# Kernel optimization log

Measured on AMD Instinct MI355X. Metric: run time of the kernel, lower is better.

Reference implementation:

```python
import jax, jax.numpy as jnp
import numpy as np

B, K = 16, 50
IN_CH, N_CLASSES, N_ANCH = 256, 80, 3
STRIDE, FSIZE, IGNORE_THRE = 8, 76, 0.7
N_CH = 5 + N_CLASSES
ANCHORS = np.array([[10,13],[16,30],[33,23],[30,61],[62,45],[59,119],[116,90],[156,198],[373,326]], np.float32)
ALL_GRID = ANCHORS / STRIDE            # all 9 anchors in grid units
ANCH_MASK = np.array([0, 1, 2])        # layer_no = 2
MASKED = ALL_GRID[ANCH_MASK]           # (3,2) anchors used by this head


def setup_inputs():
    key = jax.random.key(0)
    k1, k2, k3, k4, k5, k6 = jax.random.split(key, 6)
    xin = jax.random.normal(k1, (B, IN_CH, FSIZE, FSIZE), jnp.float32)
    cls = jax.random.randint(k2, (B, K), 0, N_CLASSES).astype(jnp.float32)
    xy = jax.random.uniform(k3, (B, K, 2), minval=0.05, maxval=0.95)
    wh = jax.random.uniform(k4, (B, K, 2), minval=0.02, maxval=0.30)
    labels = jnp.concatenate([cls[..., None], xy, wh], -1)   # (B,K,5) [cls,xc,yc,w,h]
    oc = N_ANCH * N_CH
    conv_w = jax.random.normal(k5, (oc, IN_CH), jnp.float32) * 0.01
    conv_b = jax.random.normal(k6, (oc,), jnp.float32) * 0.01
    return {"xin": xin, "labels": labels, "conv_w": conv_w, "conv_b": conv_b}


def _yolo(xin, conv_w, conv_b, labels):
    f, C = FSIZE, N_CLASSES
    # 1x1 conv == channel matmul
    raw = jnp.einsum('bchw,oc->bohw', xin, conv_w) + conv_b[None, :, None, None]
    raw = raw.reshape(B, N_ANCH, N_CH, f, f).transpose(0, 1, 3, 4, 2)  # (B,A,f,f,85)
    # sigmoid on x,y,obj,cls; w,h stay raw
    out = jnp.concatenate([jax.nn.sigmoid(raw[..., :2]), raw[..., 2:4], jax.nn.sigmoid(raw[..., 4:])], -1)

    grid = jnp.arange(f, dtype=jnp.float32)
    mw = jnp.asarray(MASKED[:, 0]); mh = jnp.asarray(MASKED[:, 1])
    px = out[..., 0] + grid[None, None, None, :]
    py = out[..., 1] + grid[None, None, :, None]
    pw = jnp.exp(out[..., 2]) * mw[None, :, None, None]
    ph = jnp.exp(out[..., 3]) * mh[None, :, None, None]
    pred = jax.lax.stop_gradient(jnp.stack([px, py, pw, ph], -1))  # detached, like torch .data

    labels = jax.lax.stop_gradient(labels)
    valid = labels.sum(-1) > 0                  # (B,K) padding rows are all-zero
    tx = labels[..., 1] * f; ty = labels[..., 2] * f
    tw = labels[..., 3] * f; th = labels[..., 4] * f
    ii = tx.astype(jnp.int32); jj = ty.astype(jnp.int32)

    # anchor matching: IoU of [0,0,w,h] truth vs [0,0,aw,ah] ref anchors (corners at origin)
    aw = jnp.asarray(ALL_GRID[:, 0]); ah = jnp.asarray(ALL_GRID[:, 1])
    inter_a = jnp.minimum(tw[..., None], aw) * jnp.minimum(th[..., None], ah)  # (B,K,9)
    iou_a = inter_a / (tw[..., None] * th[..., None] + aw * ah - inter_a)
    best_n_all = jnp.argmax(iou_a, -1)
    best_n = best_n_all % 3
    best_mask = (best_n_all == ANCH_MASK[0]) | (best_n_all == ANCH_MASK[1]) | (best_n_all == ANCH_MASK[2])

    # pred-vs-truth IoU in cxcywh form (xyxy=False)
    pa = pred.reshape(B, -1, 4)                 # (B, A*f*f, 4)
    tb = jnp.stack([tx, ty, tw, th], -1)        # (B, K, 4)
    tl = jnp.maximum(pa[:, :, None, :2] - pa[:, :, None, 2:] * 0.5, tb[:, None, :, :2] - tb[:, None, :, 2:] * 0.5)
    br = jnp.minimum(pa[:, :, None, :2] + pa[:, :, None, 2:] * 0.5, tb[:, None, :, :2] + tb[:, None, :, 2:] * 0.5)
    en = jnp.all(tl < br, -1)
    inter = jnp.prod(br - tl, -1) * en
    area_p = pa[..., 2] * pa[..., 3]; area_t = tb[..., 2] * tb[..., 3]
    iou_p = inter / (area_p[:, :, None] + area_t[:, None, :] - inter)
    iou_p = jnp.where(valid[:, None, :], iou_p, 0.0)
    ignore = (iou_p.max(-1) > IGNORE_THRE).reshape(B, N_ANCH, f, f)
    obj_mask = 1.0 - ignore.astype(jnp.float32)

    # scatter positive targets; non-selected rows routed out-of-bounds and dropped
    sel = valid & best_mask
    bb = jnp.where(sel, jnp.arange(B)[:, None], B)
    obj_mask = obj_mask.at[bb, best_n, jj, ii].set(1.0, mode='drop')
    tgt_mask = jnp.zeros((B, N_ANCH, f, f, 4 + C)).at[bb, best_n, jj, ii].set(1.0, mode='drop')
    scale = jnp.sqrt(2.0 - tw * th / (f * f))
    tgt_scale = jnp.zeros((B, N_ANCH, f, f, 2)).at[bb, best_n, jj, ii].set(
        jnp.broadcast_to(scale[..., None], (B, K, 2)), mode='drop')
    tvals = jnp.concatenate([
        (tx - ii)[..., None], (ty - jj)[..., None],
        jnp.log(tw / mw[best_n] + 1e-16)[..., None],
        jnp.log(th / mh[best_n] + 1e-16)[..., None],
        jnp.ones((B, K, 1), jnp.float32),
        jax.nn.one_hot(labels[..., 0].astype(jnp.int32), C)], -1)  # (B,K,85)
    target = jnp.zeros((B, N_ANCH, f, f, N_CH)).at[bb, best_n, jj, ii].set(tvals, mode='drop')

    oxy = out[..., :2] * tgt_mask[..., :2]
    owh = out[..., 2:4] * tgt_mask[..., 2:4] * tgt_scale
    oob = out[..., 4] * obj_mask
    ocl = out[..., 5:] * tgt_mask[..., 4:]
    txy = target[..., :2] * tgt_mask[..., :2]
    twh = target[..., 2:4] * tgt_mask[..., 2:4] * tgt_scale
    tob = target[..., 4] * obj_mask
    tcl = target[..., 5:] * tgt_mask[..., 4:]

    def bce(p, t, w=None):
        pc = jnp.clip(p, 1e-12, 1.0 - 1e-7)
        e = -(t * jnp.log(pc) + (1.0 - t) * jnp.log(1.0 - pc))
        if w is not None:
            e = e * w
        return e.sum()

    loss_xy = bce(oxy, txy, tgt_scale * tgt_scale)
    loss_wh = 0.5 * jnp.sum((owh - twh) ** 2)
    loss_obj = bce(oob, tob)
    loss_cls = bce(ocl, tcl)
    out_m = jnp.concatenate([oxy, owh, oob[..., None], ocl], -1)
    tgt_m = jnp.concatenate([txy, twh, tob[..., None], tcl], -1)
    loss_l2 = jnp.sum((out_m - tgt_m) ** 2)
    loss = loss_xy + loss_wh + loss_obj + loss_cls
    return loss, loss_xy, loss_wh, loss_obj, loss_cls, loss_l2, out_m


def reference(xin, labels, conv_w, conv_b):
    return _yolo(xin, conv_w, conv_b, labels)
```

## Files before the change

kernel.cpp:

```cpp
#include <hip/hip_runtime.h>
#include <hip/hip_bf16.h>

#define B_   16
#define K_   50
#define CIN  256
#define F_   76
#define A_   3
#define NCH  85
#define OC   255
#define HW   (F_*F_)
#define NBLK (B_*F_)
#define NCELL (A_*F_)
#define SLAB (F_*NCH)

#define WS_BIAS_F 32768
#define WS_LAB_F  33024
#define WS_PART_F 45824
#define WS_W15_F  55552

typedef __attribute__((ext_vector_type(8))) short short8;
typedef __attribute__((ext_vector_type(4))) float f32x4;

__device__ __constant__ float AW9[9] = {1.25f, 2.0f, 4.125f, 3.75f, 7.75f, 7.375f, 14.5f, 19.5f, 46.625f};
__device__ __constant__ float AH9[9] = {1.625f, 3.75f, 2.875f, 7.625f, 5.625f, 14.875f, 11.25f, 24.75f, 40.75f};

__device__ __forceinline__ unsigned short f2bf(float f) {
    union { float f; unsigned int u; } v; v.f = f;
    unsigned int r = v.u + 0x7fffu + ((v.u >> 16) & 1u);
    return (unsigned short)(r >> 16);
}
__device__ __forceinline__ float bf2f(unsigned short b) {
    union { unsigned int u; float f; } v; v.u = ((unsigned int)b) << 16;
    return v.f;
}
__device__ __forceinline__ float sigm(float r) { return 1.0f / (1.0f + __expf(-r)); }
__device__ __forceinline__ float bce_t(float p, float tv) {
    float pc = fminf(fmaxf(p, 1e-12f), 1.0f - 1e-7f);
    return -(tv * __logf(pc) + (1.0f - tv) * __logf(1.0f - pc));
}

__global__ void prep_kernel(const float* __restrict__ conv_w, const float* __restrict__ conv_b,
                            const float* __restrict__ labels, float* __restrict__ ws) {
    int bid = blockIdx.x, t = threadIdx.x;
    if (bid < 256) {
        float v = (t < OC) ? conv_w[t * CIN + bid] : 0.0f;
        ((unsigned short*)ws)[bid * 256 + t] = f2bf(v);
    } else if (bid == 256) {
        ws[WS_BIAS_F + t] = (t < OC) ? conv_b[t] : 0.0f;
    } else if (bid == 257) {
        for (int idx = t; idx < B_ * K_; idx += 256) {
            const float* L = labels + idx * 5;
            float cls = L[0], xc = L[1], yc = L[2], wl = L[3], hl = L[4];
            float ssum = cls + xc + yc + wl + hl;
            float validf = (ssum > 0.0f) ? 1.0f : 0.0f;
            float tx = xc * F_, ty = yc * F_, tw = wl * F_, th = hl * F_;
            int ii = (int)tx, jj = (int)ty;
            float tarea = tw * th;
            float best = -1.0f; int bn = 0;
            #pragma unroll
            for (int n = 0; n < 9; n++) {
                float inter = fminf(tw, AW9[n]) * fminf(th, AH9[n]);
                float iou = inter / (tarea + AW9[n] * AH9[n] - inter);
                if (iou > best) { best = iou; bn = n; }
            }
            int a = bn % 3;
            bool self = (validf != 0.0f) && (bn < 3);
            float* R = ws + WS_LAB_F + idx * 16;
            R[0] = tx; R[1] = ty; R[2] = tw; R[3] = th;
            R[4] = validf; R[5] = self ? (float)a : -1.0f; R[6] = (float)ii; R[7] = (float)jj;
            R[8] = tx - (float)ii; R[9] = ty - (float)jj;
            R[10] = __logf(tw / AW9[a] + 1e-16f);
            R[11] = __logf(th / AH9[a] + 1e-16f);
            R[12] = sqrtf(2.0f - tarea / (float)HW);
            R[13] = cls; R[14] = 0.0f; R[15] = 0.0f;
        }
    } else {
        unsigned short* wf = (unsigned short*)(ws + WS_W15_F);
        for (int idx = t; idx < 4096; idx += 256) {
            int ks = idx >> 9, lane = (idx >> 3) & 63, jj = idx & 7;
            int row = lane & 15;
            int k = ks * 32 + (lane >> 4) * 8 + jj;
            float v = 0.0f;
            if (row < 15) v = conv_w[((row / 5) * NCH + (row % 5)) * CIN + k];
            wf[idx] = f2bf(v);
        }
    }
}

__global__ __launch_bounds__(320) void fused_kernel(const float* __restrict__ xin,
                                                    const float* __restrict__ ws,
                                                    float* __restrict__ d_out,
                                                    float* __restrict__ part) {
    __shared__ float raw5S[15 * F_];
    __shared__ float4 LAB[K_ * 4];
    __shared__ int   flagS[NCELL];
    __shared__ float omvS[NCELL];
    __shared__ float xcolS[256];
    __shared__ float redS[5][5];

    const int t = threadIdx.x;
    const int w = t >> 6, lane = t & 63;
    const int b = blockIdx.x / F_;
    const int j = blockIdx.x % F_;
    const int lr = lane & 15, q = lane >> 4;
    const int col0 = (w < 4) ? (w << 4) : 60;

    if (t < K_ * 4) LAB[t] = ((const float4*)(ws + WS_LAB_F + b * (K_ * 16)))[t];

    const unsigned short* wf15 = (const unsigned short*)(ws + WS_W15_F);
    short8 afr[8];
    #pragma unroll
    for (int ks = 0; ks < 8; ks++)
        afr[ks] = *(const short8*)&wf15[(ks * 64 + lane) * 8];

    f32x4 acc = (f32x4){0.0f, 0.0f, 0.0f, 0.0f};
    const float* xbase = xin + (size_t)b * CIN * HW + j * F_ + col0 + lr;
    #pragma unroll
    for (int ks = 0; ks < 8; ks++) {
        int kb = ks * 32 + q * 8;
        float xv[8];
        #pragma unroll
        for (int jj = 0; jj < 8; jj++) xv[jj] = xbase[(size_t)(kb + jj) * HW];
        union { short8 s; __hip_bfloat162 h[4]; } u;
        #pragma unroll
        for (int p = 0; p < 4; p++)
            u.h[p] = __float22bfloat162_rn(make_float2(xv[2 * p], xv[2 * p + 1]));
        acc = __builtin_amdgcn_mfma_f32_16x16x32_bf16(afr[ks], u.s, acc, 0, 0, 0);
    }

    const float* biasg = ws + WS_BIAS_F;
    if (w < 4 || lr >= 4) {
        #pragma unroll
        for (int r = 0; r < 4; r++) {
            int row = q * 4 + r;
            if (row < 15) {
                int o = (row / 5) * NCH + (row % 5);
                raw5S[row * F_ + col0 + lr] = acc[r] + biasg[o];
            }
        }
    }
    __syncthreads();

    float lxy = 0.0f, lwh = 0.0f, lobj = 0.0f, lcls = 0.0f, l2 = 0.0f;
    if (t < NCELL) {
        int a = t / F_, i = t - a * F_;
        float x   = sigm(raw5S[(a * 5 + 0) * F_ + i]);
        float y   = sigm(raw5S[(a * 5 + 1) * F_ + i]);
        float wr  = raw5S[(a * 5 + 2) * F_ + i];
        float hr  = raw5S[(a * 5 + 3) * F_ + i];
        float obj = sigm(raw5S[(a * 5 + 4) * F_ + i]);

        float px = x + (float)i, py = y + (float)j;
        float pw = __expf(wr) * AW9[a], ph = __expf(hr) * AH9[a];
        float hpw = pw * 0.5f, hph = ph * 0.5f;
        float areap = pw * ph;
        float fa_t = (float)a, fi_t = (float)i, fj_t = (float)j;

        float maxiou = 0.0f; int mk = -1;
        #pragma unroll 2
        for (int k = 0; k < K_; k++) {
            float4 A0 = LAB[4 * k + 0];
            float4 A1 = LAB[4 * k + 1];
            float tx = A0.x, ty = A0.y, tw = A0.z, th = A0.w;
            float tlx = fmaxf(px - hpw, tx - tw * 0.5f);
            float tly = fmaxf(py - hph, ty - th * 0.5f);
            float brx = fminf(px + hpw, tx + tw * 0.5f);
            float bry = fminf(py + hph, ty + th * 0.5f);
            float iw = brx - tlx, ih = bry - tly;
            float inter = (iw > 0.0f && ih > 0.0f) ? iw * ih : 0.0f;
            float iou = __fdividef(inter, areap + tw * th - inter);
            iou = (A1.x != 0.0f) ? iou : 0.0f;
            maxiou = fmaxf(maxiou, iou);
            bool match = (A1.y == fa_t) & (A1.z == fi_t) & (A1.w == fj_t);
            mk = match ? k : mk;
        }
        float objmask = (maxiou > 0.7f) ? 0.0f : 1.0f;

        if (mk >= 0) {
            float4 B0 = LAB[4 * mk + 2];
            float4 B1 = LAB[4 * mk + 3];
            float sc = B1.x, sc2 = sc * sc;
            float txv = B0.x, tyv = B0.y, twv = B0.z, thv = B0.w;
            lxy = (bce_t(x, txv) + bce_t(y, tyv)) * sc2;
            float dw = wr - twv, dh = hr - thv;
            lwh = 0.5f * sc2 * (dw * dw + dh * dh);
            float pco = fminf(fmaxf(obj, 1e-12f), 1.0f - 1e-7f);
            lobj = -__logf(pco);
            float dx = x - txv, dy = y - tyv, dob = obj - 1.0f;
            l2 = dx * dx + dy * dy + sc2 * (dw * dw + dh * dh) + dob * dob;
            flagS[t] = mk + 1;
            omvS[t]  = obj;
        } else {
            float oo = obj * objmask;
            if (objmask != 0.0f) {
                float pco = fminf(obj, 1.0f - 1e-7f);
                lobj = -__logf(1.0f - pco);
            }
            l2 = oo * oo;
            flagS[t] = 0;
            omvS[t]  = oo;
        }
    }
    __syncthreads();

    for (int a = 0; a < A_; a++) {
        float2* dst = (float2*)(d_out + 6 + (size_t)((b * A_ + a) * F_ + j) * SLAB);
        for (int idx2 = t; idx2 < SLAB / 2; idx2 += 320) {
            int p = idx2 << 1;
            int i0 = p / NCH, c0 = p - i0 * NCH;
            int i1 = i0, c1 = c0 + 1;
            if (c1 == NCH) { i1++; c1 = 0; }
            float v0 = (c0 == 4) ? omvS[a * F_ + i0] : 0.0f;
            float v1 = (c1 == 4) ? omvS[a * F_ + i1] : 0.0f;
            dst[idx2] = make_float2(v0, v1);
        }
    }
    __threadfence_block();
    __syncthreads();

    const unsigned short* Wtg = (const unsigned short*)ws;
    for (int k = 0; k < K_; k++) {
        float4 A1 = LAB[4 * k + 1];
        int fa = (int)A1.y;
        if (fa < 0) continue;
        if ((int)A1.w != j) continue;
        int fi = (int)A1.z;
        int cell = fa * F_ + fi;
        if (flagS[cell] != k + 1) continue;

        if (t < 256) xcolS[t] = xin[((size_t)b * CIN + t) * HW + j * F_ + fi];
        __syncthreads();
        float4 B1 = LAB[4 * k + 3];
        float sc = B1.x; int cl = (int)B1.y;
        if (t < NCH) {
            float v; int chout;
            if (t < 80) {
                int o = fa * NCH + 5 + t;
                float accv = biasg[o];
                #pragma unroll 8
                for (int kk = 0; kk < 256; kk++)
                    accv += bf2f(Wtg[kk * 256 + o]) * xcolS[kk];
                float p = sigm(accv);
                float tcv = (t == cl) ? 1.0f : 0.0f;
                lcls += bce_t(p, tcv);
                float d = p - tcv;
                l2 += d * d;
                v = p; chout = 5 + t;
            } else {
                int ch = t - 80;
                float raw = raw5S[(fa * 5 + ch) * F_ + fi];
                v = (ch == 2 || ch == 3) ? raw * sc : sigm(raw);
                chout = ch;
            }
            d_out[6 + (size_t)((b * A_ + fa) * F_ + j) * SLAB + fi * NCH + chout] = v;
        }
        __syncthreads();
    }

    #pragma unroll
    for (int off = 32; off > 0; off >>= 1) {
        lxy  += __shfl_down(lxy, off);
        lwh  += __shfl_down(lwh, off);
        lobj += __shfl_down(lobj, off);
        lcls += __shfl_down(lcls, off);
        l2   += __shfl_down(l2, off);
    }
    if (lane == 0) {
        redS[w][0] = lxy; redS[w][1] = lwh; redS[w][2] = lobj;
        redS[w][3] = lcls; redS[w][4] = l2;
    }
    __syncthreads();
    if (t == 0) {
        float* P = part + (size_t)blockIdx.x * 8;
        #pragma unroll
        for (int q2 = 0; q2 < 5; q2++)
            P[q2] = redS[0][q2] + redS[1][q2] + redS[2][q2] + redS[3][q2] + redS[4][q2];
    }
}

__global__ void finish_kernel(const float* __restrict__ part, float* __restrict__ d_out) {
    int t = threadIdx.x;
    float s0 = 0, s1 = 0, s2 = 0, s3 = 0, s4 = 0;
    for (int bidx = t; bidx < NBLK; bidx += 256) {
        const float* P = part + (size_t)bidx * 8;
        s0 += P[0]; s1 += P[1]; s2 += P[2]; s3 += P[3]; s4 += P[4];
    }
    #pragma unroll
    for (int off = 32; off > 0; off >>= 1) {
        s0 += __shfl_down(s0, off); s1 += __shfl_down(s1, off);
        s2 += __shfl_down(s2, off); s3 += __shfl_down(s3, off);
        s4 += __shfl_down(s4, off);
    }
    __shared__ float red[4][5];
    if ((t & 63) == 0) {
        int w = t >> 6;
        red[w][0] = s0; red[w][1] = s1; red[w][2] = s2; red[w][3] = s3; red[w][4] = s4;
    }
    __syncthreads();
    if (t == 0) {
        float r0 = red[0][0] + red[1][0] + red[2][0] + red[3][0];
        float r1 = red[0][1] + red[1][1] + red[2][1] + red[3][1];
        float r2 = red[0][2] + red[1][2] + red[2][2] + red[3][2];
        float r3 = red[0][3] + red[1][3] + red[2][3] + red[3][3];
        float r4 = red[0][4] + red[1][4] + red[2][4] + red[3][4];
        d_out[0] = r0 + r1 + r2 + r3;
        d_out[1] = r0; d_out[2] = r1; d_out[3] = r2; d_out[4] = r3; d_out[5] = r4;
    }
}

extern "C" void kernel_launch(void* const* d_in, const int* in_sizes, int n_in,
                              void* d_out, int out_size, void* d_ws, size_t ws_size,
                              hipStream_t stream) {
    const float* xin    = (const float*)d_in[0];
    const float* labels = (const float*)d_in[1];
    const float* conv_w = (const float*)d_in[2];
    const float* conv_b = (const float*)d_in[3];
    float* out  = (float*)d_out;
    float* ws   = (float*)d_ws;
    float* part = ws + WS_PART_F;

    prep_kernel<<<259, 256, 0, stream>>>(conv_w, conv_b, labels, ws);
    fused_kernel<<<NBLK, 320, 0, stream>>>(xin, ws, out, part);
    finish_kernel<<<1, 256, 0, stream>>>(part, out);
}
```

Before: 212.4 us.

## Stage x row tile in LDS as bf16 with coalesced loads; simplify output zero-fill

```diff
diff --git a/kernel.cpp b/kernel.cpp
--- a/kernel.cpp
+++ b/kernel.cpp
@@ -12,6 +12,7 @@
 #define NBLK (B_*F_)
 #define NCELL (A_*F_)
 #define SLAB (F_*NCH)
+#define XPAD 78
 
 #define WS_BIAS_F 32768
 #define WS_LAB_F  33024
@@ -91,10 +92,10 @@
                                                     const float* __restrict__ ws,
                                                     float* __restrict__ d_out,
                                                     float* __restrict__ part) {
+    __shared__ unsigned short xS[256 * XPAD];
     __shared__ float raw5S[15 * F_];
     __shared__ float4 LAB[K_ * 4];
     __shared__ int   flagS[NCELL];
-    __shared__ float omvS[NCELL];
     __shared__ float xcolS[256];
     __shared__ float redS[5][5];
 
@@ -105,26 +106,43 @@
     const int lr = lane & 15, q = lane >> 4;
     const int col0 = (w < 4) ? (w << 4) : 60;
 
-    if (t < K_ * 4) LAB[t] = ((const float4*)(ws + WS_LAB_F + b * (K_ * 16)))[t];
-
     const unsigned short* wf15 = (const unsigned short*)(ws + WS_W15_F);
     short8 afr[8];
     #pragma unroll
     for (int ks = 0; ks < 8; ks++)
         afr[ks] = *(const short8*)&wf15[(ks * 64 + lane) * 8];
 
+    {
+        const float* xrow = xin + (size_t)b * CIN * HW + j * F_;
+        #pragma unroll 4
+        for (int it = 0; it < 16; ++it) {
+            int fidx = t + it * 320;
+            if (fidx < 256 * 19) {
+                int c = fidx / 19, pg = fidx - c * 19;
+                float4 v = *(const float4*)(xrow + (size_t)c * HW + pg * 4);
+                __hip_bfloat162 h0 = __float22bfloat162_rn(make_float2(v.x, v.y));
+                __hip_bfloat162 h1 = __float22bfloat162_rn(make_float2(v.z, v.w));
+                unsigned int* dst = (unsigned int*)&xS[c * XPAD + pg * 4];
+                dst[0] = *(unsigned int*)&h0;
+                dst[1] = *(unsigned int*)&h1;
+            }
+        }
+    }
+    if (t < K_ * 4) LAB[t] = ((const float4*)(ws + WS_LAB_F + b * (K_ * 16)))[t];
+    __syncthreads();
+
+    const int pp = col0 + lr;
     f32x4 acc = (f32x4){0.0f, 0.0f, 0.0f, 0.0f};
-    const float* xbase = xin + (size_t)b * CIN * HW + j * F_ + col0 + lr;
     #pragma unroll
     for (int ks = 0; ks < 8; ks++) {
         int kb = ks * 32 + q * 8;
-        float xv[8];
+        unsigned short ev[8];
         #pragma unroll
-        for (int jj = 0; jj < 8; jj++) xv[jj] = xbase[(size_t)(kb + jj) * HW];
-        union { short8 s; __hip_bfloat162 h[4]; } u;
+        for (int jj = 0; jj < 8; jj++) ev[jj] = xS[(kb + jj) * XPAD + pp];
+        union { short8 s; unsigned int d[4]; } u;
         #pragma unroll
-        for (int p = 0; p < 4; p++)
-            u.h[p] = __float22bfloat162_rn(make_float2(xv[2 * p], xv[2 * p + 1]));
+        for (int p2 = 0; p2 < 4; p2++)
+            u.d[p2] = (unsigned int)ev[2 * p2] | ((unsigned int)ev[2 * p2 + 1] << 16);
         acc = __builtin_amdgcn_mfma_f32_16x16x32_bf16(afr[ks], u.s, acc, 0, 0, 0);
     }
 
@@ -142,6 +160,7 @@
     __syncthreads();
 
     float lxy = 0.0f, lwh = 0.0f, lobj = 0.0f, lcls = 0.0f, l2 = 0.0f;
+    float omv = 0.0f;
     if (t < NCELL) {
         int a = t / F_, i = t - a * F_;
         float x   = sigm(raw5S[(a * 5 + 0) * F_ + i]);
@@ -189,7 +208,7 @@
             float dx = x - txv, dy = y - tyv, dob = obj - 1.0f;
             l2 = dx * dx + dy * dy + sc2 * (dw * dw + dh * dh) + dob * dob;
             flagS[t] = mk + 1;
-            omvS[t]  = obj;
+            omv = obj;
         } else {
             float oo = obj * objmask;
             if (objmask != 0.0f) {
@@ -198,22 +217,23 @@
             }
             l2 = oo * oo;
             flagS[t] = 0;
-            omvS[t]  = oo;
-        }
-    }
-    __syncthreads();
-
+            omv = oo;
+        }
+    }
+    __syncthreads();
+
+    #pragma unroll
     for (int a = 0; a < A_; a++) {
         float2* dst = (float2*)(d_out + 6 + (size_t)((b * A_ + a) * F_ + j) * SLAB);
-        for (int idx2 = t; idx2 < SLAB / 2; idx2 += 320) {
-            int p = idx2 << 1;
-            int i0 = p / NCH, c0 = p - i0 * NCH;
-            int i1 = i0, c1 = c0 + 1;
-            if (c1 == NCH) { i1++; c1 = 0; }
-            float v0 = (c0 == 4) ? omvS[a * F_ + i0] : 0.0f;
-            float v1 = (c1 == 4) ? omvS[a * F_ + i1] : 0.0f;
-            dst[idx2] = make_float2(v0, v1);
-        }
+        for (int idx2 = t; idx2 < SLAB / 2; idx2 += 320)
+            dst[idx2] = make_float2(0.0f, 0.0f);
+    }
+    __threadfence_block();
+    __syncthreads();
+
+    if (t < NCELL) {
+        int a = t / F_, i = t - a * F_;
+        d_out[6 + (size_t)((b * A_ + a) * F_ + j) * SLAB + i * NCH + 4] = omv;
     }
     __threadfence_block();
     __syncthreads();
```

Result: slower. 227.7 us (+7.2%).

## Pre-transpose input to channel-last bf16 in workspace and vectorize slab writes

Applied to the files above, without the earlier changes.

```diff
diff --git a/kernel.cpp b/kernel.cpp
--- a/kernel.cpp
+++ b/kernel.cpp
@@ -17,6 +17,10 @@
 #define WS_LAB_F  33024
 #define WS_PART_F 45824
 #define WS_W15_F  55552
+#define WS_XT_F   57600
+#define XT_FLOATS (11829248u)
+
+#define NTILE 91
 
 typedef __attribute__((ext_vector_type(8))) short short8;
 typedef __attribute__((ext_vector_type(4))) float f32x4;
@@ -39,8 +43,11 @@
     return -(tv * __logf(pc) + (1.0f - tv) * __logf(1.0f - pc));
 }
 
+template<bool XTP>
 __global__ void prep_kernel(const float* __restrict__ conv_w, const float* __restrict__ conv_b,
-                            const float* __restrict__ labels, float* __restrict__ ws) {
+                            const float* __restrict__ labels, const float* __restrict__ xin,
+                            float* __restrict__ ws) {
+    __shared__ float tS[64][65];
     int bid = blockIdx.x, t = threadIdx.x;
     if (bid < 256) {
         float v = (t < OC) ? conv_w[t * CIN + bid] : 0.0f;
@@ -74,7 +81,7 @@
             R[12] = sqrtf(2.0f - tarea / (float)HW);
             R[13] = cls; R[14] = 0.0f; R[15] = 0.0f;
         }
-    } else {
+    } else if (bid == 258) {
         unsigned short* wf = (unsigned short*)(ws + WS_W15_F);
         for (int idx = t; idx < 4096; idx += 256) {
             int ks = idx >> 9, lane = (idx >> 3) & 63, jj = idx & 7;
@@ -84,9 +91,44 @@
             if (row < 15) v = conv_w[((row / 5) * NCH + (row % 5)) * CIN + k];
             wf[idx] = f2bf(v);
         }
-    }
-}
-
+    } else if (XTP) {
+        int bid2 = bid - 259;
+        int bt = bid2 / NTILE, tile = bid2 - bt * NTILE;
+        int hw0 = tile * 64;
+        int npos = HW - hw0; if (npos > 64) npos = 64;
+        unsigned short* xT = (unsigned short*)(ws + WS_XT_F);
+        const float* xb = xin + (size_t)bt * CIN * HW + hw0;
+        const int c_l = t >> 2, g = t & 3;
+        for (int cc = 0; cc < 4; cc++) {
+            const float* src = xb + (size_t)(cc * 64 + c_l) * HW;
+            #pragma unroll
+            for (int k2 = 0; k2 < 4; k2++) {
+                int p_l = 4 * g + 16 * k2;
+                if (p_l < npos) {
+                    float4 v = *(const float4*)(src + p_l);
+                    tS[c_l][p_l] = v.x; tS[c_l][p_l + 1] = v.y;
+                    tS[c_l][p_l + 2] = v.z; tS[c_l][p_l + 3] = v.w;
+                }
+            }
+            __syncthreads();
+            if (c_l < npos) {
+                unsigned int ow[8];
+                #pragma unroll
+                for (int u = 0; u < 8; u++) {
+                    __hip_bfloat162 h = __float22bfloat162_rn(
+                        make_float2(tS[g * 16 + 2 * u][c_l], tS[g * 16 + 2 * u + 1][c_l]));
+                    ow[u] = *(unsigned int*)&h;
+                }
+                uint4* dst = (uint4*)(xT + ((size_t)bt * HW + hw0 + c_l) * 256 + cc * 64 + g * 16);
+                dst[0] = make_uint4(ow[0], ow[1], ow[2], ow[3]);
+                dst[1] = make_uint4(ow[4], ow[5], ow[6], ow[7]);
+            }
+            __syncthreads();
+        }
+    }
+}
+
+template<bool XT>
 __global__ __launch_bounds__(320) void fused_kernel(const float* __restrict__ xin,
                                                     const float* __restrict__ ws,
                                                     float* __restrict__ d_out,
@@ -114,18 +156,28 @@
         afr[ks] = *(const short8*)&wf15[(ks * 64 + lane) * 8];
 
     f32x4 acc = (f32x4){0.0f, 0.0f, 0.0f, 0.0f};
-    const float* xbase = xin + (size_t)b * CIN * HW + j * F_ + col0 + lr;
-    #pragma unroll
-    for (int ks = 0; ks < 8; ks++) {
-        int kb = ks * 32 + q * 8;
-        float xv[8];
+    if (XT) {
+        const unsigned short* xTp = (const unsigned short*)(ws + WS_XT_F)
+                                  + ((size_t)(b * HW + j * F_ + col0 + lr)) * 256;
         #pragma unroll
-        for (int jj = 0; jj < 8; jj++) xv[jj] = xbase[(size_t)(kb + jj) * HW];
-        union { short8 s; __hip_bfloat162 h[4]; } u;
+        for (int ks = 0; ks < 8; ks++) {
+            short8 bfr = *(const short8*)(xTp + ks * 32 + q * 8);
+            acc = __builtin_amdgcn_mfma_f32_16x16x32_bf16(afr[ks], bfr, acc, 0, 0, 0);
+        }
+    } else {
+        const float* xbase = xin + (size_t)b * CIN * HW + j * F_ + col0 + lr;
         #pragma unroll
-        for (int p = 0; p < 4; p++)
-            u.h[p] = __float22bfloat162_rn(make_float2(xv[2 * p], xv[2 * p + 1]));
-        acc = __builtin_amdgcn_mfma_f32_16x16x32_bf16(afr[ks], u.s, acc, 0, 0, 0);
+        for (int ks = 0; ks < 8; ks++) {
+            int kb = ks * 32 + q * 8;
+            float xv[8];
+            #pragma unroll
+            for (int jj = 0; jj < 8; jj++) xv[jj] = xbase[(size_t)(kb + jj) * HW];
+            union { short8 s; __hip_bfloat162 h[4]; } u;
+            #pragma unroll
+            for (int p = 0; p < 4; p++)
+                u.h[p] = __float22bfloat162_rn(make_float2(xv[2 * p], xv[2 * p + 1]));
+            acc = __builtin_amdgcn_mfma_f32_16x16x32_bf16(afr[ks], u.s, acc, 0, 0, 0);
+        }
     }
 
     const float* biasg = ws + WS_BIAS_F;
@@ -203,19 +255,21 @@
     }
     __syncthreads();
 
+    #pragma unroll
     for (int a = 0; a < A_; a++) {
-        float2* dst = (float2*)(d_out + 6 + (size_t)((b * A_ + a) * F_ + j) * SLAB);
-        for (int idx2 = t; idx2 < SLAB / 2; idx2 += 320) {
-            int p = idx2 << 1;
-            int i0 = p / NCH, c0 = p - i0 * NCH;
-            int i1 = i0, c1 = c0 + 1;
-            if (c1 == NCH) { i1++; c1 = 0; }
-            float v0 = (c0 == 4) ? omvS[a * F_ + i0] : 0.0f;
-            float v1 = (c1 == 4) ? omvS[a * F_ + i1] : 0.0f;
-            dst[idx2] = make_float2(v0, v1);
-        }
-    }
-    __threadfence_block();
+        float* slab = d_out + 6 + (size_t)((b * A_ + a) * F_ + j) * SLAB;
+        const float* om = &omvS[a * F_];
+        if (t == 0) { slab[0] = 0.0f; slab[1] = 0.0f; }
+        if (t == 1) { slab[6458] = 0.0f; slab[6459] = 0.0f; }
+        float4* dst4 = (float4*)(slab + 2);
+        for (int n = t; n < 1614; n += 320) {
+            int f0 = 2 + 4 * n;
+            int p = f0 / 85, r = f0 - 85 * p;
+            float4 v = make_float4(0.0f, 0.0f, 0.0f, 0.0f);
+            if (r >= 1 && r <= 4) ((float*)&v)[4 - r] = om[p];
+            dst4[n] = v;
+        }
+    }
     __syncthreads();
 
     const unsigned short* Wtg = (const unsigned short*)ws;
@@ -319,7 +373,13 @@
     float* ws   = (float*)d_ws;
     float* part = ws + WS_PART_F;
 
-    prep_kernel<<<259, 256, 0, stream>>>(conv_w, conv_b, labels, ws);
-    fused_kernel<<<NBLK, 320, 0, stream>>>(xin, ws, out, part);
+    const size_t need = ((size_t)WS_XT_F + (size_t)XT_FLOATS) * 4u;
+    if (ws_size >= need) {
+        prep_kernel<true><<<259 + B_ * NTILE, 256, 0, stream>>>(conv_w, conv_b, labels, xin, ws);
+        fused_kernel<true><<<NBLK, 320, 0, stream>>>(xin, ws, out, part);
+    } else {
+        prep_kernel<false><<<259, 256, 0, stream>>>(conv_w, conv_b, labels, xin, ws);
+        fused_kernel<false><<<NBLK, 320, 0, stream>>>(xin, ws, out, part);
+    }
     finish_kernel<<<1, 256, 0, stream>>>(part, out);
 }
```

Result: slower. 224.8 us (+5.8%).

## Split 15-channel conv into a separate FP32 kernel and vectorize output slab writes

Applied to the files above, without the earlier changes.

```diff
diff --git a/kernel.cpp b/kernel.cpp
--- a/kernel.cpp
+++ b/kernel.cpp
@@ -17,6 +17,13 @@
 #define WS_LAB_F  33024
 #define WS_PART_F 45824
 #define WS_W15_F  55552
+#define WS_W15P_F 57600
+#define WS_B15_F  61696
+#define WS_RAW5_F 61712
+#define RAW5_FLOATS (B_*15*HW)
+
+#define CTILE 128
+#define NT2   46
 
 typedef __attribute__((ext_vector_type(8))) short short8;
 typedef __attribute__((ext_vector_type(4))) float f32x4;
@@ -74,7 +81,7 @@
             R[12] = sqrtf(2.0f - tarea / (float)HW);
             R[13] = cls; R[14] = 0.0f; R[15] = 0.0f;
         }
-    } else {
+    } else if (bid == 258) {
         unsigned short* wf = (unsigned short*)(ws + WS_W15_F);
         for (int idx = t; idx < 4096; idx += 256) {
             int ks = idx >> 9, lane = (idx >> 3) & 63, jj = idx & 7;
@@ -84,9 +91,46 @@
             if (row < 15) v = conv_w[((row / 5) * NCH + (row % 5)) * CIN + k];
             wf[idx] = f2bf(v);
         }
-    }
-}
-
+    } else {
+        for (int idx = t; idx < 4096; idx += 256) {
+            int c = idx >> 4, r = idx & 15;
+            float v = 0.0f;
+            if (r < 15) v = conv_w[((r / 5) * NCH + (r % 5)) * CIN + c];
+            ws[WS_W15P_F + idx] = v;
+        }
+        if (t < 16) ws[WS_B15_F + t] = (t < 15) ? conv_b[(t / 5) * NCH + (t % 5)] : 0.0f;
+    }
+}
+
+__global__ __launch_bounds__(128) void conv_kernel(const float* __restrict__ xin,
+                                                   const float* __restrict__ ws,
+                                                   float* __restrict__ raw5g) {
+    const int t = threadIdx.x;
+    const int bt = blockIdx.x / NT2, tile = blockIdx.x - bt * NT2;
+    const int p = tile * CTILE + t;
+    const bool ok = p < HW;
+    const float* xp = xin + (size_t)bt * CIN * HW + (ok ? p : 0);
+    const float* Wp = ws + WS_W15P_F;
+
+    float acc[15];
+    #pragma unroll
+    for (int r = 0; r < 15; r++) acc[r] = ws[WS_B15_F + r];
+
+    #pragma unroll 4
+    for (int c = 0; c < 256; c++) {
+        float xv = xp[(size_t)c * HW];
+        #pragma unroll
+        for (int r = 0; r < 15; r++) acc[r] = fmaf(xv, Wp[c * 16 + r], acc[r]);
+    }
+
+    if (ok) {
+        float* dst = raw5g + (size_t)bt * 15 * HW + p;
+        #pragma unroll
+        for (int r = 0; r < 15; r++) dst[(size_t)r * HW] = acc[r];
+    }
+}
+
+template<bool R5>
 __global__ __launch_bounds__(320) void fused_kernel(const float* __restrict__ xin,
                                                     const float* __restrict__ ws,
                                                     float* __restrict__ d_out,
@@ -102,40 +146,46 @@
     const int w = t >> 6, lane = t & 63;
     const int b = blockIdx.x / F_;
     const int j = blockIdx.x % F_;
-    const int lr = lane & 15, q = lane >> 4;
-    const int col0 = (w < 4) ? (w << 4) : 60;
 
     if (t < K_ * 4) LAB[t] = ((const float4*)(ws + WS_LAB_F + b * (K_ * 16)))[t];
-
-    const unsigned short* wf15 = (const unsigned short*)(ws + WS_W15_F);
-    short8 afr[8];
-    #pragma unroll
-    for (int ks = 0; ks < 8; ks++)
-        afr[ks] = *(const short8*)&wf15[(ks * 64 + lane) * 8];
-
-    f32x4 acc = (f32x4){0.0f, 0.0f, 0.0f, 0.0f};
-    const float* xbase = xin + (size_t)b * CIN * HW + j * F_ + col0 + lr;
-    #pragma unroll
-    for (int ks = 0; ks < 8; ks++) {
-        int kb = ks * 32 + q * 8;
-        float xv[8];
-        #pragma unroll
-        for (int jj = 0; jj < 8; jj++) xv[jj] = xbase[(size_t)(kb + jj) * HW];
-        union { short8 s; __hip_bfloat162 h[4]; } u;
-        #pragma unroll
-        for (int p = 0; p < 4; p++)
-            u.h[p] = __float22bfloat162_rn(make_float2(xv[2 * p], xv[2 * p + 1]));
-        acc = __builtin_amdgcn_mfma_f32_16x16x32_bf16(afr[ks], u.s, acc, 0, 0, 0);
-    }
-
     const float* biasg = ws + WS_BIAS_F;
-    if (w < 4 || lr >= 4) {
-        #pragma unroll
-        for (int r = 0; r < 4; r++) {
-            int row = q * 4 + r;
-            if (row < 15) {
-                int o = (row / 5) * NCH + (row % 5);
-                raw5S[row * F_ + col0 + lr] = acc[r] + biasg[o];
+
+    if (R5) {
+        const float* r5 = ws + WS_RAW5_F + (size_t)b * 15 * HW + j * F_;
+        for (int idx = t; idx < 15 * F_; idx += 320) {
+            int row = idx / F_, i = idx - row * F_;
+            raw5S[idx] = r5[row * HW + i];
+        }
+    } else {
+        const int lr = lane & 15, q = lane >> 4;
+        const int col0 = (w < 4) ? (w << 4) : 60;
+        const unsigned short* wf15 = (const unsigned short*)(ws + WS_W15_F);
+        short8 afr[8];
+        #pragma unroll
+        for (int ks = 0; ks < 8; ks++)
+            afr[ks] = *(const short8*)&wf15[(ks * 64 + lane) * 8];
+        f32x4 acc = (f32x4){0.0f, 0.0f, 0.0f, 0.0f};
+        const float* xbase = xin + (size_t)b * CIN * HW + j * F_ + col0 + lr;
+        #pragma unroll
+        for (int ks = 0; ks < 8; ks++) {
+            int kb = ks * 32 + q * 8;
+            float xv[8];
+            #pragma unroll
+            for (int jj = 0; jj < 8; jj++) xv[jj] = xbase[(size_t)(kb + jj) * HW];
+            union { short8 s; __hip_bfloat162 h[4]; } u;
+            #pragma unroll
+            for (int p = 0; p < 4; p++)
+                u.h[p] = __float22bfloat162_rn(make_float2(xv[2 * p], xv[2 * p + 1]));
+            acc = __builtin_amdgcn_mfma_f32_16x16x32_bf16(afr[ks], u.s, acc, 0, 0, 0);
+        }
+        if (w < 4 || lr >= 4) {
+            #pragma unroll
+            for (int r = 0; r < 4; r++) {
+                int row = q * 4 + r;
+                if (row < 15) {
+                    int o = (row / 5) * NCH + (row % 5);
+                    raw5S[row * F_ + col0 + lr] = acc[r] + biasg[o];
+                }
             }
         }
     }
@@ -203,19 +253,21 @@
     }
     __syncthreads();
 
+    #pragma unroll
     for (int a = 0; a < A_; a++) {
-        float2* dst = (float2*)(d_out + 6 + (size_t)((b * A_ + a) * F_ + j) * SLAB);
-        for (int idx2 = t; idx2 < SLAB / 2; idx2 += 320) {
-            int p = idx2 << 1;
-            int i0 = p / NCH, c0 = p - i0 * NCH;
-            int i1 = i0, c1 = c0 + 1;
-            if (c1 == NCH) { i1++; c1 = 0; }
-            float v0 = (c0 == 4) ? omvS[a * F_ + i0] : 0.0f;
-            float v1 = (c1 == 4) ? omvS[a * F_ + i1] : 0.0f;
-            dst[idx2] = make_float2(v0, v1);
-        }
-    }
-    __threadfence_block();
+        float* slab = d_out + 6 + (size_t)((b * A_ + a) * F_ + j) * SLAB;
+        const float* om = &omvS[a * F_];
+        if (t == 0) { slab[0] = 0.0f; slab[1] = 0.0f; }
+        if (t == 1) { slab[6458] = 0.0f; slab[6459] = 0.0f; }
+        float4* dst4 = (float4*)(slab + 2);
+        for (int n = t; n < 1614; n += 320) {
+            int f0 = 2 + 4 * n;
+            int p = f0 / 85, r = f0 - 85 * p;
+            float4 v = make_float4(0.0f, 0.0f, 0.0f, 0.0f);
+            if (r >= 1 && r <= 4) ((float*)&v)[4 - r] = om[p];
+            dst4[n] = v;
+        }
+    }
     __syncthreads();
 
     const unsigned short* Wtg = (const unsigned short*)ws;
@@ -319,7 +371,13 @@
     float* ws   = (float*)d_ws;
     float* part = ws + WS_PART_F;
 
-    prep_kernel<<<259, 256, 0, stream>>>(conv_w, conv_b, labels, ws);
-    fused_kernel<<<NBLK, 320, 0, stream>>>(xin, ws, out, part);
+    prep_kernel<<<260, 256, 0, stream>>>(conv_w, conv_b, labels, ws);
+    const size_t need = ((size_t)WS_RAW5_F + (size_t)RAW5_FLOATS) * 4u;
+    if (ws_size >= need) {
+        conv_kernel<<<B_ * NT2, CTILE, 0, stream>>>(xin, ws, ws + WS_RAW5_F);
+        fused_kernel<true><<<NBLK, 320, 0, stream>>>(xin, ws, out, part);
+    } else {
+        fused_kernel<false><<<NBLK, 320, 0, stream>>>(xin, ws, out, part);
+    }
     finish_kernel<<<1, 256, 0, stream>>>(part, out);
 }
```

After: 245.7 us. 15.7% more time.
